# Performance work log

Measured on AMD Instinct MI355X. Metric: run time of the kernel, lower is better.

Reference implementation:

```python
import jax, jax.numpy as jnp
import numpy as np

B, T = 256, 1024
V, E, H = 27, 64, 128


def setup_inputs() -> dict:
    key = jax.random.key(0)
    ks = jax.random.split(key, 8)
    return {
        "x": jax.random.randint(ks[0], (B, T), 0, V, dtype=jnp.int32),
        "emb": jax.random.normal(ks[1], (V, E), dtype=jnp.float32) * 0.02,
        "wx0": jax.random.normal(ks[2], (E, 4 * H), dtype=jnp.float32) * 0.01,
        "wh0": jax.random.normal(ks[3], (H, 4 * H), dtype=jnp.float32) * 0.01,
        "b0": jnp.zeros((4 * H,), dtype=jnp.float32),
        "wx1": jax.random.normal(ks[4], (H, 4 * H), dtype=jnp.float32) * 0.01,
        "wh1": jax.random.normal(ks[5], (H, 4 * H), dtype=jnp.float32) * 0.01,
        "b1": jnp.zeros((4 * H,), dtype=jnp.float32),
        "why": jax.random.normal(ks[6], (H, V), dtype=jnp.float32),
        "by": jnp.zeros((V,), dtype=jnp.float32),
    }


def _cell(xt, h_prev, c_prev, wx, wh, b):
    # gates: [B, 4H]; chunk order matches torch .chunk(4): f, i, g, o
    gates = xt @ wx + h_prev @ wh + b
    ft, it, gt, ot = jnp.split(gates, 4, axis=1)
    c_t = jax.nn.sigmoid(ft) * c_prev + jax.nn.sigmoid(it) * jnp.tanh(gt)
    h_t = jnp.tanh(c_t) * jax.nn.sigmoid(ot)
    return h_t, c_t


def reference(x, emb, wx0, wh0, b0, wx1, wh1, b1, why, by):
    Bx = x.shape[0]
    xe = emb[x]                       # [B, T, E]
    xe = jnp.swapaxes(xe, 0, 1)       # [T, B, E] for scan over time
    h0 = jnp.zeros((Bx, H), jnp.float32)
    c0 = jnp.zeros((Bx, H), jnp.float32)
    h1 = jnp.zeros((Bx, H), jnp.float32)
    c1 = jnp.zeros((Bx, H), jnp.float32)

    def step(carry, xt):
        h0, c0, h1, c1 = carry
        h0, c0 = _cell(xt, h0, c0, wx0, wh0, b0)   # layer 0
        h1, c1 = _cell(h0, h1, c1, wx1, wh1, b1)   # layer 1 (dropout off in eval)
        yt = h1 @ why + by                         # [B, V]
        return (h0, c0, h1, c1), yt

    _, ys = jax.lax.scan(step, (h0, c0, h1, c1), xe)  # ys: [T, B, V]
    return jnp.swapaxes(ys, 0, 1)                     # [B, T, V]
```

## Files before the change

kernel.cpp:

```cpp
#include <hip/hip_runtime.h>


#define B_  256
#define T_  1024
#define V_  27
#define E_  64
#define H_  128
#define G4  512
#define TPITCH 528

typedef float v2f __attribute__((ext_vector_type(2)));

__device__ __forceinline__ v2f mkv2(float a, float b) { v2f r; r.x = a; r.y = b; return r; }

template <int CTRL>
__device__ __forceinline__ float dppmov(float v) {
    return __int_as_float(__builtin_amdgcn_update_dpp(
               0, __float_as_int(v), CTRL, 0xF, 0xF, true));
}
__device__ __forceinline__ float qsum(float v) {
    v += dppmov<0xB1>(v);
    v += dppmov<0x4E>(v);
    return v;
}
__device__ __forceinline__ float tanh_fast(float y) {
    const float t = __expf(2.f * y);
    return fmaf(-2.f, __builtin_amdgcn_rcpf(t + 1.f), 1.f);
}

#define REPEAT16(M) M(0) M(1) M(2) M(3) M(4) M(5) M(6) M(7) \
                    M(8) M(9) M(10) M(11) M(12) M(13) M(14) M(15)

#define DECLW(K) v2f wf##K, wi##K, wg##K, wo##K;
#define LOADW(K) { const float* r0 = wmat + (size_t)(kb + 2*(K)) * G4; \
                   wf##K = mkv2(r0[p],          r0[G4 + p]); \
                   wi##K = mkv2(r0[H_ + p],     r0[G4 + H_ + p]); \
                   wg##K = mkv2(r0[2*H_ + p],   r0[G4 + 2*H_ + p]); \
                   wo##K = mkv2(r0[3*H_ + p],   r0[G4 + 3*H_ + p]); }
#define PINW(K) asm("" : "+v"(wf##K), "+v"(wi##K), "+v"(wg##K), "+v"(wo##K));
#define FMAP(K, HA, HB) { const v2f h2 = mkv2(HA, HB); \
    sf2 = __builtin_elementwise_fma(h2, wf##K, sf2); \
    si2 = __builtin_elementwise_fma(h2, wi##K, si2); \
    sg2 = __builtin_elementwise_fma(h2, wg##K, sg2); \
    so2 = __builtin_elementwise_fma(h2, wo##K, so2); }

#define FMABODY \
    v2f sf2 = mkv2(0.f, 0.f), si2 = sf2, sg2 = sf2, so2 = sf2; \
    FMAP(0,  v0.x, v0.y) FMAP(1,  v0.z, v0.w) \
    FMAP(2,  v1.x, v1.y) FMAP(3,  v1.z, v1.w) \
    FMAP(4,  v2.x, v2.y) FMAP(5,  v2.z, v2.w) \
    FMAP(6,  v3.x, v3.y) FMAP(7,  v3.z, v3.w) \
    FMAP(8,  v4.x, v4.y) FMAP(9,  v4.z, v4.w) \
    FMAP(10, v5.x, v5.y) FMAP(11, v5.z, v5.w) \
    FMAP(12, v6.x, v6.y) FMAP(13, v6.z, v6.w) \
    FMAP(14, v7.x, v7.y) FMAP(15, v7.z, v7.w)

__global__ __launch_bounds__(G4)
void build_table0(const float* __restrict__ emb,
                  const float* __restrict__ wx0,
                  const float* __restrict__ b0,
                  float* __restrict__ table0)
{
    const int v = blockIdx.x;
    const int j = threadIdx.x;
    __shared__ float e[E_];
    if (j < E_) e[j] = emb[v * E_ + j];
    __syncthreads();
    float s = b0[j];
#pragma unroll 8
    for (int k = 0; k < E_; ++k) s += e[k] * wx0[k * G4 + j];
    const int r = j & (H_ - 1), gate = j >> 7;
    table0[v * TPITCH + gate * 132 + r] = s;
}

__global__ __launch_bounds__(512, 2)
void lstm_l0_chunk(const int* __restrict__ x,
                   const float* __restrict__ table0,
                   const float* __restrict__ wh0,
                   float* __restrict__ h0st, float* __restrict__ c0st,
                   float* __restrict__ h0buf,
                   int t0, int TC)
{
    const int j = threadIdx.x;
    const int p = j >> 2;
    const int e = j & 3;
    const int b = blockIdx.x;
    const int kb = 32 * e;

    __shared__ __align__(16) float hP[2][4][36];
    __shared__ __align__(16) float tabS[V_ * TPITCH];

    const float* wmat = wh0;
    REPEAT16(DECLW)
    REPEAT16(LOADW)
    for (int i = j; i < V_ * TPITCH; i += 512) tabS[i] = table0[i];
    if (j < H_) hP[0][j >> 5][j & 31] = h0st[b * H_ + j];
    float c = c0st[b * H_ + p];
    float hh = 0.f;
    __syncthreads();

    const int* xb = x + (size_t)b * T_ + t0;
    float* hob = h0buf + (size_t)b * TC * H_;
    const float A = (e == 2) ? 2.f : 1.f;

    int idx = xb[0];
    for (int t = 0; t < TC; ++t) {
        REPEAT16(PINW)
        const int idxn = (t + 1 < TC) ? xb[t + 1] : 0;
        const float tv = tabS[idx * TPITCH + e * 132 + p];

        const float4* hb4 = reinterpret_cast<const float4*>(&hP[t & 1][e][0]);
        const float4 v0 = hb4[0], v1 = hb4[1], v2 = hb4[2], v3 = hb4[3],
                     v4 = hb4[4], v5 = hb4[5], v6 = hb4[6], v7 = hb4[7];
        FMABODY
        const float sf = qsum(sf2.x + sf2.y);
        const float si = qsum(si2.x + si2.y);
        const float sg = qsum(sg2.x + sg2.y);
        const float so = qsum(so2.x + so2.y);

        float val = (e == 0) ? sf : (e == 1) ? si : (e == 2) ? sg : so;
        val += tv;
        const float tz  = __expf(A * val);
        const float act = fmaf(-A, __builtin_amdgcn_rcpf(tz + 1.f), 1.f);

        const float iv = dppmov<0x39>(act);
        const float gv = dppmov<0x4E>(act);
        const float ov = dppmov<0x93>(act);
        c  = fmaf(act, c, iv * gv);
        hh = tanh_fast(c) * ov;

        if (e == 0) {
            hP[(t + 1) & 1][p >> 5][p & 31] = hh;
            hob[(size_t)t * H_ + p] = hh;
        }
        idx = idxn;
        __syncthreads();
    }
    if (e == 0) { h0st[b * H_ + p] = hh; c0st[b * H_ + p] = c; }
}

__global__ __launch_bounds__(G4, 2)
void gemm_xg1(const float* __restrict__ h0buf,
              const float* __restrict__ wx1,
              const float* __restrict__ b1,
              float* __restrict__ xg1)
{
    const int j  = threadIdx.x;
    const size_t m0 = (size_t)blockIdx.x * 64;
    const int c  = j & 127;
    const int rg = j >> 7;

    __shared__ __align__(16) float aT[64 * 132];

#pragma unroll
    for (int i = 0; i < 4; ++i) {
        const int e  = i * G4 + j;
        const int r  = e >> 5;
        const int k4 = e & 31;
        const float4 v = *reinterpret_cast<const float4*>(&h0buf[(m0 + r) * H_ + k4 * 4]);
        *reinterpret_cast<float4*>(&aT[r * 132 + k4 * 4]) = v;
    }
    __syncthreads();

    float acc[4][16];
#pragma unroll
    for (int cc = 0; cc < 4; ++cc)
#pragma unroll
        for (int rr = 0; rr < 16; ++rr) acc[cc][rr] = 0.f;

    for (int k4 = 0; k4 < 32; ++k4) {
        float bv[4][4];
#pragma unroll
        for (int kk = 0; kk < 4; ++kk)
#pragma unroll
            for (int cc = 0; cc < 4; ++cc)
                bv[kk][cc] = wx1[(size_t)(k4 * 4 + kk) * G4 + cc * 128 + c];
#pragma unroll
        for (int rr = 0; rr < 16; ++rr) {
            const float4 av = *reinterpret_cast<const float4*>(&aT[(rg * 16 + rr) * 132 + k4 * 4]);
#pragma unroll
            for (int cc = 0; cc < 4; ++cc) {
                acc[cc][rr] = fmaf(av.x, bv[0][cc], acc[cc][rr]);
                acc[cc][rr] = fmaf(av.y, bv[1][cc], acc[cc][rr]);
                acc[cc][rr] = fmaf(av.z, bv[2][cc], acc[cc][rr]);
                acc[cc][rr] = fmaf(av.w, bv[3][cc], acc[cc][rr]);
            }
        }
    }

    float b1v[4];
#pragma unroll
    for (int cc = 0; cc < 4; ++cc) b1v[cc] = b1[cc * 128 + c];
#pragma unroll
    for (int rr = 0; rr < 16; ++rr) {
        const size_t row = m0 + rg * 16 + rr;
#pragma unroll
        for (int cc = 0; cc < 4; ++cc)
            xg1[row * G4 + cc * 128 + c] = acc[cc][rr] + b1v[cc];
    }
}

__global__ __launch_bounds__(512, 2)
void lstm_l1_chunk(const float* __restrict__ xg1,
                   const float* __restrict__ wh1,
                   float* __restrict__ h1st, float* __restrict__ c1st,
                   float* __restrict__ h1buf,
                   int TC)
{
    const int j = threadIdx.x;
    const int p = j >> 2;
    const int e = j & 3;
    const int b = blockIdx.x;
    const int kb = 32 * e;

    __shared__ __align__(16) float hP[2][4][36];

    const float* wmat = wh1;
    REPEAT16(DECLW)
    REPEAT16(LOADW)
    if (j < H_) hP[0][j >> 5][j & 31] = h1st[b * H_ + j];
    float c = c1st[b * H_ + p];
    float hh = 0.f;
    __syncthreads();

    const float* xgb = xg1 + (size_t)b * TC * G4;
    float* hob = h1buf + (size_t)b * TC * H_;
    const float A = (e == 2) ? 2.f : 1.f;
    const int xcol = e * H_ + p;

    float xv = xgb[xcol];
    for (int t = 0; t < TC; ++t) {
        REPEAT16(PINW)
        const float xvn = (t + 1 < TC) ? xgb[(size_t)(t + 1) * G4 + xcol] : 0.f;

        const float4* hb4 = reinterpret_cast<const float4*>(&hP[t & 1][e][0]);
        const float4 v0 = hb4[0], v1 = hb4[1], v2 = hb4[2], v3 = hb4[3],
                     v4 = hb4[4], v5 = hb4[5], v6 = hb4[6], v7 = hb4[7];
        FMABODY
        const float sf = qsum(sf2.x + sf2.y);
        const float si = qsum(si2.x + si2.y);
        const float sg = qsum(sg2.x + sg2.y);
        const float so = qsum(so2.x + so2.y);

        float val = (e == 0) ? sf : (e == 1) ? si : (e == 2) ? sg : so;
        val += xv;
        const float tz  = __expf(A * val);
        const float act = fmaf(-A, __builtin_amdgcn_rcpf(tz + 1.f), 1.f);

        const float iv = dppmov<0x39>(act);
        const float gv = dppmov<0x4E>(act);
        const float ov = dppmov<0x93>(act);
        c  = fmaf(act, c, iv * gv);
        hh = tanh_fast(c) * ov;

        if (e == 0) {
            hP[(t + 1) & 1][p >> 5][p & 31] = hh;
            hob[(size_t)t * H_ + p] = hh;
        }
        xv = xvn;
        __syncthreads();
    }
    if (e == 0) { h1st[b * H_ + p] = hh; c1st[b * H_ + p] = c; }
}

__global__ __launch_bounds__(256)
void proj_y(const float* __restrict__ h1buf,
            const float* __restrict__ why,
            const float* __restrict__ by,
            float* __restrict__ out,
            int t0, int TC)
{
    const int tid = threadIdx.x;
    const int b   = blockIdx.x;

    __shared__ __align__(16) float whyS[V_][H_];
    __shared__ float byS[V_];
    __shared__ float yS[256][29];

    for (int e = tid; e < V_ * H_; e += 256) {
        const int v = e / H_, k = e - v * H_;
        whyS[v][k] = why[k * V_ + v];
    }
    if (tid < V_) byS[tid] = by[tid];
    __syncthreads();

    const float* hb  = h1buf + (size_t)b * TC * H_;
    float* outb      = out + ((size_t)b * T_ + t0) * V_;

    for (int tt0 = 0; tt0 < TC; tt0 += 256) {
        const int tt = tt0 + tid;
        if (tt < TC) {
            float acc[V_];
#pragma unroll
            for (int v = 0; v < V_; ++v) acc[v] = byS[v];
            const float4* hr = reinterpret_cast<const float4*>(hb + (size_t)tt * H_);
#pragma unroll 4
            for (int k4 = 0; k4 < 32; ++k4) {
                const float4 hv = hr[k4];
#pragma unroll
                for (int v = 0; v < V_; ++v) {
                    const float4 wv = *reinterpret_cast<const float4*>(&whyS[v][k4 * 4]);
                    acc[v] = fmaf(hv.x, wv.x,
                             fmaf(hv.y, wv.y,
                             fmaf(hv.z, wv.z,
                             fmaf(hv.w, wv.w, acc[v]))));
                }
            }
#pragma unroll
            for (int v = 0; v < V_; ++v) yS[tid][v] = acc[v];
        }
        __syncthreads();
        const int nrow = (TC - tt0 < 256) ? (TC - tt0) : 256;
        const int n = nrow * V_;
        float* od = outb + (size_t)tt0 * V_;
        for (int i = tid; i < n; i += 256) {
            const int r = i / V_, v = i - r * V_;
            od[i] = yS[r][v];
        }
        __syncthreads();
    }
}

__global__ __launch_bounds__(G4, 1)
void lstm_persist(const int* __restrict__ x,
                  const float* __restrict__ table0,
                  const float* __restrict__ wh0,
                  const float* __restrict__ wx1,
                  const float* __restrict__ wh1,
                  const float* __restrict__ b1,
                  const float* __restrict__ why,
                  const float* __restrict__ by,
                  float* __restrict__ out)
{
    const int j  = threadIdx.x;
    const int bb = blockIdx.x * 2;

    __shared__ float h0s[2][H_], c0s[2][H_], h1s[2][H_], c1s[2][H_];
    __shared__ float hcat[2][2 * H_];
    __shared__ float g0s[2][G4], g1s[2][G4];
    __shared__ float whyS[H_ * V_];
    __shared__ float b1S[G4];
    __shared__ float byS[V_];
    __shared__ float pb[2][V_][8];

    for (int i = j; i < H_ * V_; i += G4) whyS[i] = why[i];
    b1S[j] = b1[j];
    if (j < V_) byS[j] = by[j];
    if (j < H_) {
        h0s[0][j] = 0.f; h0s[1][j] = 0.f; c0s[0][j] = 0.f; c0s[1][j] = 0.f;
        h1s[0][j] = 0.f; h1s[1][j] = 0.f; c1s[0][j] = 0.f; c1s[1][j] = 0.f;
    }
    __syncthreads();

    const int* xA = x + (size_t)(bb + 0) * T_;
    const int* xB = x + (size_t)(bb + 1) * T_;
    float* outA = out + (size_t)(bb + 0) * T_ * V_;
    float* outB = out + (size_t)(bb + 1) * T_ * V_;

    const int tix = (j >> 7) * 132 + (j & (H_ - 1));

    for (int t = 0; t < T_; ++t) {
        const int ia = xA[t];
        const int ib = xB[t];
        float aA = table0[ia * TPITCH + tix];
        float aB = table0[ib * TPITCH + tix];
#pragma unroll 8
        for (int k = 0; k < H_; ++k) {
            const float w = wh0[k * G4 + j];
            aA += h0s[0][k] * w;
            aB += h0s[1][k] * w;
        }
        g0s[0][j] = aA; g0s[1][j] = aB;
        __syncthreads();

        if (j < 2 * H_) {
            const int gi = j >> 7, r = j & (H_ - 1);
            const float f  = 1.f / (1.f + expf(-g0s[gi][r]));
            const float i_ = 1.f / (1.f + expf(-g0s[gi][H_ + r]));
            const float g  = tanhf(g0s[gi][2 * H_ + r]);
            const float o  = 1.f / (1.f + expf(-g0s[gi][3 * H_ + r]));
            const float c  = f * c0s[gi][r] + i_ * g;
            c0s[gi][r] = c;
            const float h = tanhf(c) * o;
            h0s[gi][r] = h;
            hcat[gi][r] = h;
            hcat[gi][H_ + r] = h1s[gi][r];
        }
        __syncthreads();

        float bA = b1S[j];
        float bB = bA;
#pragma unroll 8
        for (int k = 0; k < H_; ++k) {
            const float w = wx1[k * G4 + j];
            bA += hcat[0][k] * w;
            bB += hcat[1][k] * w;
        }
#pragma unroll 8
        for (int k = 0; k < H_; ++k) {
            const float w = wh1[k * G4 + j];
            bA += hcat[0][H_ + k] * w;
            bB += hcat[1][H_ + k] * w;
        }
        g1s[0][j] = bA; g1s[1][j] = bB;
        __syncthreads();

        if (j < 2 * H_) {
            const int gi = j >> 7, r = j & (H_ - 1);
            const float f  = 1.f / (1.f + expf(-g1s[gi][r]));
            const float i_ = 1.f / (1.f + expf(-g1s[gi][H_ + r]));
            const float g  = tanhf(g1s[gi][2 * H_ + r]);
            const float o  = 1.f / (1.f + expf(-g1s[gi][3 * H_ + r]));
            const float c  = f * c1s[gi][r] + i_ * g;
            c1s[gi][r] = c;
            h1s[gi][r] = tanhf(c) * o;
        }
        __syncthreads();

        if (j < 2 * V_ * 8) {
            int q = j;
            const int gi = (q >= V_ * 8) ? 1 : 0;
            q -= gi * V_ * 8;
            const int v = q >> 3, kk = q & 7;
            float pv = 0.f;
#pragma unroll
            for (int k = kk * 16; k < kk * 16 + 16; ++k)
                pv += h1s[gi][k] * whyS[k * V_ + v];
            pb[gi][v][kk] = pv;
        }
        __syncthreads();

        if (j < 2 * V_) {
            const int gi = (j >= V_) ? 1 : 0;
            const int v  = j - gi * V_;
            float s = byS[v];
#pragma unroll
            for (int q = 0; q < 8; ++q) s += pb[gi][v][q];
            (gi ? outB : outA)[t * V_ + v] = s;
        }
        __syncthreads();
    }
}

extern "C" void kernel_launch(void* const* d_in, const int* in_sizes, int n_in,
                              void* d_out, int out_size, void* d_ws, size_t ws_size,
                              hipStream_t stream)
{
    const int*   x   = (const int*)  d_in[0];
    const float* emb = (const float*)d_in[1];
    const float* wx0 = (const float*)d_in[2];
    const float* wh0 = (const float*)d_in[3];
    const float* b0  = (const float*)d_in[4];
    const float* wx1 = (const float*)d_in[5];
    const float* wh1 = (const float*)d_in[6];
    const float* b1  = (const float*)d_in[7];
    const float* why = (const float*)d_in[8];
    const float* by  = (const float*)d_in[9];
    float* out = (float*)d_out;
    float* wsf = (float*)d_ws;

    const size_t tabF   = (size_t)V_ * TPITCH;
    const size_t stateF = (size_t)4 * B_ * H_;

    int TC = 0;
    for (int tc = T_; tc >= 32; tc >>= 1) {
        const size_t need = (tabF + stateF + (size_t)B_ * tc * (H_ + G4 + H_)) * 4;
        if (need <= ws_size) { TC = tc; break; }
    }

    float* table0 = wsf;
    build_table0<<<dim3(V_), dim3(G4), 0, stream>>>(emb, wx0, b0, table0);

    if (TC == 0) {
        lstm_persist<<<dim3(B_ / 2), dim3(G4), 0, stream>>>(
            x, table0, wh0, wx1, wh1, b1, why, by, out);
        return;
    }

    float* h0st   = wsf + tabF;
    float* c0st   = h0st + (size_t)B_ * H_;
    float* h1st   = c0st + (size_t)B_ * H_;
    float* c1st   = h1st + (size_t)B_ * H_;
    float* h0buf  = c1st + (size_t)B_ * H_;
    float* xg1buf = h0buf + (size_t)B_ * TC * H_;
    float* h1buf  = xg1buf + (size_t)B_ * TC * G4;

    (void)hipMemsetAsync(h0st, 0, stateF * sizeof(float), stream);

    const int NC = T_ / TC;
    for (int c = 0; c < NC; ++c) {
        const int t0 = c * TC;
        lstm_l0_chunk<<<dim3(B_), dim3(512), 0, stream>>>(
            x, table0, wh0, h0st, c0st, h0buf, t0, TC);
        gemm_xg1<<<dim3(4 * TC), dim3(G4), 0, stream>>>(
            h0buf, wx1, b1, xg1buf);
        lstm_l1_chunk<<<dim3(B_), dim3(512), 0, stream>>>(
            xg1buf, wh1, h1st, c1st, h1buf, TC);
        proj_y<<<dim3(B_), dim3(256), 0, stream>>>(
            h1buf, why, by, out, t0, TC);
    }
}
```

Baseline: 1.856 ms.

## Remap LSTM recurrent threads to 8-way K split with two rows per group

Both recurrent LSTM kernels now give each group of 8 lanes two hidden units across all four gates, with the hidden-state dot product split 8 ways (16 k per lane) instead of 4 ways. This halves the per-lane LDS read of h each step, and partial sums are reduced with a three-step DPP butterfly that includes a half-row mirror. The packed FMAs are written as inline v_pk_fma_f32 asm. The layer-0 kernel also stops staging the 27×528 gate table in LDS and gathers it directly from global memory one step ahead. In exchange there are twice as many cross-lane reductions per step plus extra selects, and each table lookup now goes through the cache rather than LDS.

```diff
diff --git a/kernel.cpp b/kernel.cpp
--- a/kernel.cpp
+++ b/kernel.cpp
@@ -10,6 +10,7 @@
 #define TPITCH 528
 
 typedef float v2f __attribute__((ext_vector_type(2)));
+typedef float v4f __attribute__((ext_vector_type(4)));
 
 __device__ __forceinline__ v2f mkv2(float a, float b) { v2f r; r.x = a; r.y = b; return r; }
 
@@ -18,9 +19,10 @@
     return __int_as_float(__builtin_amdgcn_update_dpp(
                0, __float_as_int(v), CTRL, 0xF, 0xF, true));
 }
-__device__ __forceinline__ float qsum(float v) {
+__device__ __forceinline__ float sum8(float v) {
     v += dppmov<0xB1>(v);
     v += dppmov<0x4E>(v);
+    v += dppmov<0x141>(v);
     return v;
 }
 __device__ __forceinline__ float tanh_fast(float y) {
@@ -28,32 +30,25 @@
     return fmaf(-2.f, __builtin_amdgcn_rcpf(t + 1.f), 1.f);
 }
 
-#define REPEAT16(M) M(0) M(1) M(2) M(3) M(4) M(5) M(6) M(7) \
-                    M(8) M(9) M(10) M(11) M(12) M(13) M(14) M(15)
-
-#define DECLW(K) v2f wf##K, wi##K, wg##K, wo##K;
+#define REPEAT8(M) M(0) M(1) M(2) M(3) M(4) M(5) M(6) M(7)
+
+#define DECLW(K) v2f wAf##K, wAi##K, wAg##K, wAo##K, wBf##K, wBi##K, wBg##K, wBo##K;
 #define LOADW(K) { const float* r0 = wmat + (size_t)(kb + 2*(K)) * G4; \
-                   wf##K = mkv2(r0[p],          r0[G4 + p]); \
-                   wi##K = mkv2(r0[H_ + p],     r0[G4 + H_ + p]); \
-                   wg##K = mkv2(r0[2*H_ + p],   r0[G4 + 2*H_ + p]); \
-                   wo##K = mkv2(r0[3*H_ + p],   r0[G4 + 3*H_ + p]); }
-#define PINW(K) asm("" : "+v"(wf##K), "+v"(wi##K), "+v"(wg##K), "+v"(wo##K));
-#define FMAP(K, HA, HB) { const v2f h2 = mkv2(HA, HB); \
-    sf2 = __builtin_elementwise_fma(h2, wf##K, sf2); \
-    si2 = __builtin_elementwise_fma(h2, wi##K, si2); \
-    sg2 = __builtin_elementwise_fma(h2, wg##K, sg2); \
-    so2 = __builtin_elementwise_fma(h2, wo##K, so2); }
-
-#define FMABODY \
-    v2f sf2 = mkv2(0.f, 0.f), si2 = sf2, sg2 = sf2, so2 = sf2; \
-    FMAP(0,  v0.x, v0.y) FMAP(1,  v0.z, v0.w) \
-    FMAP(2,  v1.x, v1.y) FMAP(3,  v1.z, v1.w) \
-    FMAP(4,  v2.x, v2.y) FMAP(5,  v2.z, v2.w) \
-    FMAP(6,  v3.x, v3.y) FMAP(7,  v3.z, v3.w) \
-    FMAP(8,  v4.x, v4.y) FMAP(9,  v4.z, v4.w) \
-    FMAP(10, v5.x, v5.y) FMAP(11, v5.z, v5.w) \
-    FMAP(12, v6.x, v6.y) FMAP(13, v6.z, v6.w) \
-    FMAP(14, v7.x, v7.y) FMAP(15, v7.z, v7.w)
+                   const float* r1 = r0 + G4; \
+                   wAf##K = mkv2(r0[rA],          r1[rA]); \
+                   wAi##K = mkv2(r0[H_ + rA],     r1[H_ + rA]); \
+                   wAg##K = mkv2(r0[2*H_ + rA],   r1[2*H_ + rA]); \
+                   wAo##K = mkv2(r0[3*H_ + rA],   r1[3*H_ + rA]); \
+                   wBf##K = mkv2(r0[rB],          r1[rB]); \
+                   wBi##K = mkv2(r0[H_ + rB],     r1[H_ + rB]); \
+                   wBg##K = mkv2(r0[2*H_ + rB],   r1[2*H_ + rB]); \
+                   wBo##K = mkv2(r0[3*H_ + rB],   r1[3*H_ + rB]); }
+
+#define PKFMA(ACC, H2, W2) asm("v_pk_fma_f32 %0, %1, %2, %0" : "+v"(ACC) : "v"(H2), "v"(W2));
+#define FMAK(K, H2) { PKFMA(aAf, H2, wAf##K) PKFMA(aAi, H2, wAi##K) \
+                      PKFMA(aAg, H2, wAg##K) PKFMA(aAo, H2, wAo##K) \
+                      PKFMA(aBf, H2, wBf##K) PKFMA(aBi, H2, wBi##K) \
+                      PKFMA(aBg, H2, wBg##K) PKFMA(aBo, H2, wBo##K) }
 
 __global__ __launch_bounds__(G4)
 void build_table0(const float* __restrict__ emb,
@@ -81,45 +76,68 @@
                    float* __restrict__ h0buf,
                    int t0, int TC)
 {
-    const int j = threadIdx.x;
-    const int p = j >> 2;
-    const int e = j & 3;
-    const int b = blockIdx.x;
-    const int kb = 32 * e;
-
-    __shared__ __align__(16) float hP[2][4][36];
-    __shared__ __align__(16) float tabS[V_ * TPITCH];
+    const int j  = threadIdx.x;
+    const int rg = j >> 3;
+    const int q  = j & 7;
+    const int b  = blockIdx.x;
+    const int kb = 16 * q;
+    const int rA = 2 * rg, rB = 2 * rg + 1;
+    const int g  = q & 3;
+    const int rr = 2 * rg + (q >> 2);
+
+    __shared__ __align__(16) float hP[2][8][20];
 
     const float* wmat = wh0;
-    REPEAT16(DECLW)
-    REPEAT16(LOADW)
-    for (int i = j; i < V_ * TPITCH; i += 512) tabS[i] = table0[i];
-    if (j < H_) hP[0][j >> 5][j & 31] = h0st[b * H_ + j];
-    float c = c0st[b * H_ + p];
+    REPEAT8(DECLW)
+    REPEAT8(LOADW)
+    if (j < H_) hP[0][j >> 4][j & 15] = h0st[b * H_ + j];
+    float c = c0st[b * H_ + rr];
     float hh = 0.f;
     __syncthreads();
 
     const int* xb = x + (size_t)b * T_ + t0;
     float* hob = h0buf + (size_t)b * TC * H_;
-    const float A = (e == 2) ? 2.f : 1.f;
-
-    int idx = xb[0];
+    const float A = (g == 2) ? 2.f : 1.f;
+    const int toff = g * 132 + rr;
+    const bool q0 = (q & 1), q1 = (q & 2), q2 = (q & 4);
+
+    float tv = table0[xb[0] * TPITCH + toff];
     for (int t = 0; t < TC; ++t) {
-        REPEAT16(PINW)
         const int idxn = (t + 1 < TC) ? xb[t + 1] : 0;
-        const float tv = tabS[idx * TPITCH + e * 132 + p];
-
-        const float4* hb4 = reinterpret_cast<const float4*>(&hP[t & 1][e][0]);
-        const float4 v0 = hb4[0], v1 = hb4[1], v2 = hb4[2], v3 = hb4[3],
-                     v4 = hb4[4], v5 = hb4[5], v6 = hb4[6], v7 = hb4[7];
-        FMABODY
-        const float sf = qsum(sf2.x + sf2.y);
-        const float si = qsum(si2.x + si2.y);
-        const float sg = qsum(sg2.x + sg2.y);
-        const float so = qsum(so2.x + so2.y);
-
-        float val = (e == 0) ? sf : (e == 1) ? si : (e == 2) ? sg : so;
-        val += tv;
+
+        const v4f* hb4 = reinterpret_cast<const v4f*>(&hP[t & 1][q][0]);
+        const v4f u0 = hb4[0], u1 = hb4[1], u2 = hb4[2], u3 = hb4[3];
+        const v2f h0 = __builtin_shufflevector(u0, u0, 0, 1);
+        const v2f h1 = __builtin_shufflevector(u0, u0, 2, 3);
+        const v2f h2 = __builtin_shufflevector(u1, u1, 0, 1);
+        const v2f h3 = __builtin_shufflevector(u1, u1, 2, 3);
+        const v2f h4 = __builtin_shufflevector(u2, u2, 0, 1);
+        const v2f h5 = __builtin_shufflevector(u2, u2, 2, 3);
+        const v2f h6 = __builtin_shufflevector(u3, u3, 0, 1);
+        const v2f h7 = __builtin_shufflevector(u3, u3, 2, 3);
+
+        v2f aAf = mkv2(0.f, 0.f), aAi = aAf, aAg = aAf, aAo = aAf,
+            aBf = aAf, aBi = aAf, aBg = aAf, aBo = aAf;
+        FMAK(0, h0) FMAK(1, h1) FMAK(2, h2) FMAK(3, h3)
+        FMAK(4, h4) FMAK(5, h5) FMAK(6, h6) FMAK(7, h7)
+
+        const float sAf = sum8(aAf.x + aAf.y);
+        const float sAi = sum8(aAi.x + aAi.y);
+        const float sAg = sum8(aAg.x + aAg.y);
+        const float sAo = sum8(aAo.x + aAo.y);
+        const float sBf = sum8(aBf.x + aBf.y);
+        const float sBi = sum8(aBi.x + aBi.y);
+        const float sBg = sum8(aBg.x + aBg.y);
+        const float sBo = sum8(aBo.x + aBo.y);
+
+        const float s0 = q0 ? sAi : sAf;
+        const float s1 = q0 ? sAo : sAg;
+        const float s2 = q0 ? sBi : sBf;
+        const float s3 = q0 ? sBo : sBg;
+        const float s4 = q1 ? s1 : s0;
+        const float s5 = q1 ? s3 : s2;
+        const float val = (q2 ? s5 : s4) + tv;
+
         const float tz  = __expf(A * val);
         const float act = fmaf(-A, __builtin_amdgcn_rcpf(tz + 1.f), 1.f);
 
@@ -129,14 +147,14 @@
         c  = fmaf(act, c, iv * gv);
         hh = tanh_fast(c) * ov;
 
-        if (e == 0) {
-            hP[(t + 1) & 1][p >> 5][p & 31] = hh;
-            hob[(size_t)t * H_ + p] = hh;
-        }
-        idx = idxn;
-        __syncthreads();
-    }
-    if (e == 0) { h0st[b * H_ + p] = hh; c0st[b * H_ + p] = c; }
+        if (g == 0) {
+            hP[(t + 1) & 1][rr >> 4][rr & 15] = hh;
+            hob[(size_t)t * H_ + rr] = hh;
+        }
+        tv = table0[idxn * TPITCH + toff];
+        __syncthreads();
+    }
+    if (g == 0) { h0st[b * H_ + rr] = hh; c0st[b * H_ + rr] = c; }
 }
 
 __global__ __launch_bounds__(G4, 2)
@@ -207,43 +225,68 @@
                    float* __restrict__ h1buf,
                    int TC)
 {
-    const int j = threadIdx.x;
-    const int p = j >> 2;
-    const int e = j & 3;
-    const int b = blockIdx.x;
-    const int kb = 32 * e;
-
-    __shared__ __align__(16) float hP[2][4][36];
+    const int j  = threadIdx.x;
+    const int rg = j >> 3;
+    const int q  = j & 7;
+    const int b  = blockIdx.x;
+    const int kb = 16 * q;
+    const int rA = 2 * rg, rB = 2 * rg + 1;
+    const int g  = q & 3;
+    const int rr = 2 * rg + (q >> 2);
+
+    __shared__ __align__(16) float hP[2][8][20];
 
     const float* wmat = wh1;
-    REPEAT16(DECLW)
-    REPEAT16(LOADW)
-    if (j < H_) hP[0][j >> 5][j & 31] = h1st[b * H_ + j];
-    float c = c1st[b * H_ + p];
+    REPEAT8(DECLW)
+    REPEAT8(LOADW)
+    if (j < H_) hP[0][j >> 4][j & 15] = h1st[b * H_ + j];
+    float c = c1st[b * H_ + rr];
     float hh = 0.f;
     __syncthreads();
 
     const float* xgb = xg1 + (size_t)b * TC * G4;
     float* hob = h1buf + (size_t)b * TC * H_;
-    const float A = (e == 2) ? 2.f : 1.f;
-    const int xcol = e * H_ + p;
+    const float A = (g == 2) ? 2.f : 1.f;
+    const int xcol = g * H_ + rr;
+    const bool q0 = (q & 1), q1 = (q & 2), q2 = (q & 4);
 
     float xv = xgb[xcol];
     for (int t = 0; t < TC; ++t) {
-        REPEAT16(PINW)
         const float xvn = (t + 1 < TC) ? xgb[(size_t)(t + 1) * G4 + xcol] : 0.f;
 
-        const float4* hb4 = reinterpret_cast<const float4*>(&hP[t & 1][e][0]);
-        const float4 v0 = hb4[0], v1 = hb4[1], v2 = hb4[2], v3 = hb4[3],
-                     v4 = hb4[4], v5 = hb4[5], v6 = hb4[6], v7 = hb4[7];
-        FMABODY
-        const float sf = qsum(sf2.x + sf2.y);
-        const float si = qsum(si2.x + si2.y);
-        const float sg = qsum(sg2.x + sg2.y);
-        const float so = qsum(so2.x + so2.y);
-
-        float val = (e == 0) ? sf : (e == 1) ? si : (e == 2) ? sg : so;
-        val += xv;
+        const v4f* hb4 = reinterpret_cast<const v4f*>(&hP[t & 1][q][0]);
+        const v4f u0 = hb4[0], u1 = hb4[1], u2 = hb4[2], u3 = hb4[3];
+        const v2f h0 = __builtin_shufflevector(u0, u0, 0, 1);
+        const v2f h1 = __builtin_shufflevector(u0, u0, 2, 3);
+        const v2f h2 = __builtin_shufflevector(u1, u1, 0, 1);
+        const v2f h3 = __builtin_shufflevector(u1, u1, 2, 3);
+        const v2f h4 = __builtin_shufflevector(u2, u2, 0, 1);
+        const v2f h5 = __builtin_shufflevector(u2, u2, 2, 3);
+        const v2f h6 = __builtin_shufflevector(u3, u3, 0, 1);
+        const v2f h7 = __builtin_shufflevector(u3, u3, 2, 3);
+
+        v2f aAf = mkv2(0.f, 0.f), aAi = aAf, aAg = aAf, aAo = aAf,
+            aBf = aAf, aBi = aAf, aBg = aAf, aBo = aAf;
+        FMAK(0, h0) FMAK(1, h1) FMAK(2, h2) FMAK(3, h3)
+        FMAK(4, h4) FMAK(5, h5) FMAK(6, h6) FMAK(7, h7)
+
+        const float sAf = sum8(aAf.x + aAf.y);
+        const float sAi = sum8(aAi.x + aAi.y);
+        const float sAg = sum8(aAg.x + aAg.y);
+        const float sAo = sum8(aAo.x + aAo.y);
+        const float sBf = sum8(aBf.x + aBf.y);
+        const float sBi = sum8(aBi.x + aBi.y);
+        const float sBg = sum8(aBg.x + aBg.y);
+        const float sBo = sum8(aBo.x + aBo.y);
+
+        const float s0 = q0 ? sAi : sAf;
+        const float s1 = q0 ? sAo : sAg;
+        const float s2 = q0 ? sBi : sBf;
+        const float s3 = q0 ? sBo : sBg;
+        const float s4 = q1 ? s1 : s0;
+        const float s5 = q1 ? s3 : s2;
+        const float val = (q2 ? s5 : s4) + xv;
+
         const float tz  = __expf(A * val);
         const float act = fmaf(-A, __builtin_amdgcn_rcpf(tz + 1.f), 1.f);
 
@@ -253,14 +296,14 @@
         c  = fmaf(act, c, iv * gv);
         hh = tanh_fast(c) * ov;
 
-        if (e == 0) {
-            hP[(t + 1) & 1][p >> 5][p & 31] = hh;
-            hob[(size_t)t * H_ + p] = hh;
+        if (g == 0) {
+            hP[(t + 1) & 1][rr >> 4][rr & 15] = hh;
+            hob[(size_t)t * H_ + rr] = hh;
         }
         xv = xvn;
         __syncthreads();
     }
-    if (e == 0) { h1st[b * H_ + p] = hh; c1st[b * H_ + p] = c; }
+    if (g == 0) { h1st[b * H_ + rr] = hh; c1st[b * H_ + rr] = c; }
 }
 
 __global__ __launch_bounds__(256)
@@ -418,10 +461,10 @@
         __syncthreads();
 
         if (j < 2 * V_ * 8) {
-            int q = j;
-            const int gi = (q >= V_ * 8) ? 1 : 0;
-            q -= gi * V_ * 8;
-            const int v = q >> 3, kk = q & 7;
+            int qq = j;
+            const int gi = (qq >= V_ * 8) ? 1 : 0;
+            qq -= gi * V_ * 8;
+            const int v = qq >> 3, kk = qq & 7;
             float pv = 0.f;
 #pragma unroll
             for (int k = kk * 16; k < kk * 16 + 16; ++k)
@@ -435,7 +478,7 @@
             const int v  = j - gi * V_;
             float s = byS[v];
 #pragma unroll
-            for (int q = 0; q < 8; ++q) s += pb[gi][v][q];
+            for (int qq = 0; qq < 8; ++qq) s += pb[gi][v][qq];
             (gi ? outB : outA)[t * V_ + v] = s;
         }
         __syncthreads();
```

New measurement: 2.131 ms. 1.15x slower.
